# Kernel optimization log

Measured on AMD Instinct MI355X. Metric: run time of the kernel, lower is better.

Reference implementation:

```python
import jax, jax.numpy as jnp
import numpy as np

N = 1024  # hidden_state
L = 16384  # sequence length


def setup_inputs() -> dict:
    key = jax.random.key(0)
    kA, kB, kC, kd, kX = jax.random.split(key, 5)
    # kaiming_normal_ with nonlinearity='linear': std = 1/sqrt(fan_in) = 1/sqrt(N)
    A = jax.random.normal(kA, (N, N), dtype=jnp.float32) / jnp.sqrt(jnp.float32(N))
    # nn.init.normal_(B, std=(1/N)**0.5)
    B = jax.random.normal(kB, (N, 1), dtype=jnp.float32) / jnp.sqrt(jnp.float32(N))
    # nn.init.normal_(C, std=1.0)
    C = jax.random.normal(kC, (1, N), dtype=jnp.float32)
    D = jnp.ones((1,), dtype=jnp.float32)
    # uniform in [log(min_delta), log(max_delta)]
    log_delta = jax.random.uniform(kd, (1,), dtype=jnp.float32,
                                   minval=jnp.log(1e-3), maxval=jnp.log(1e-1))
    X = jax.random.normal(kX, (L,), dtype=jnp.float32)
    return {"X": X, "A": A, "B": B, "C": C, "D": D, "log_delta": log_delta}


def _discretize(A, B, log_delta):
    n = A.shape[0]
    I = jnp.eye(n, dtype=A.dtype)
    d = jnp.exp(log_delta)  # (1,) broadcasts
    A1 = I - d * 0.5 * A
    A2 = I + d * 0.5 * A
    A1_inv = jnp.linalg.inv(A1)
    dA = A1_inv @ A2                 # (N, N) bilinear (Tustin) discretization
    dB = (A1_inv @ (d * B))[:, 0]    # (N,)
    return dA, dB


def reference(X, A, B, C, D, log_delta):
    """S4 RNN-mode forward: linear state-space recurrence + skip connection."""
    dA, dB = _discretize(A, B, log_delta)
    c = C[0]  # (N,)

    def step(h, x):
        # h_k = dA @ h_{k-1} + dB * x_k ; y_k = C @ h_k
        h = dA @ h + dB * x
        return h, c @ h

    h0 = jnp.zeros((A.shape[0],), dtype=A.dtype)  # cache_h_k starts at zeros
    _, ys = jax.lax.scan(step, h0, X)             # ys: (L,)
    return ys + D * X                              # skip = D * X
```

## Files before the change

### kernel.cpp

```cpp
#include <hip/hip_runtime.h>
#include <math.h>

#define N1 1024
#define NN2 (N1*N1)
#define LL 16384

__global__ __launch_bounds__(256) void k_scale(const float* __restrict__ A,
                                               const float* __restrict__ logd,
                                               float* __restrict__ e) {
    int i = blockIdx.x * 256 + threadIdx.x;
    float d = expf(logd[0]);
    e[i] = 0.5f * d * A[i];
}

__global__ __launch_bounds__(256) void k_add(const float* __restrict__ a,
                                             const float* __restrict__ b,
                                             float* __restrict__ o) {
    int i = blockIdx.x * 256 + threadIdx.x;
    o[i] = a[i] + b[i];
}

__global__ __launch_bounds__(256) void k_mmk(const float* __restrict__ A,
                                             const float* __restrict__ B,
                                             float* __restrict__ part) {
    __shared__ float As[32][68];
    __shared__ float Bs[32][68];
    int t = threadIdx.x;
    int m0 = blockIdx.y * 64, n0 = blockIdx.x * 64;
    int kz = blockIdx.z * 512;
    int tm = (t & 15) * 4, tn = (t >> 4) * 4;
    int lmA = t >> 2, lkA = (t & 3) * 8;
    int kbB = t >> 3, nbB = (t & 7) * 8;
    const float* Ap = A + (size_t)(m0 + lmA) * N1 + kz + lkA;
    const float* Bp = B + (size_t)(kz + kbB) * N1 + n0 + nbB;

    float4 pa0 = *(const float4*)(Ap);
    float4 pa1 = *(const float4*)(Ap + 4);
    float4 pb0 = *(const float4*)(Bp);
    float4 pb1 = *(const float4*)(Bp + 4);

    float acc[4][4];
#pragma unroll
    for (int i = 0; i < 4; ++i)
#pragma unroll
        for (int j = 0; j < 4; ++j) acc[i][j] = 0.f;

    for (int k0 = 0; k0 < 512; k0 += 32) {
        As[lkA + 0][lmA] = pa0.x; As[lkA + 1][lmA] = pa0.y;
        As[lkA + 2][lmA] = pa0.z; As[lkA + 3][lmA] = pa0.w;
        As[lkA + 4][lmA] = pa1.x; As[lkA + 5][lmA] = pa1.y;
        As[lkA + 6][lmA] = pa1.z; As[lkA + 7][lmA] = pa1.w;
        *(float4*)&Bs[kbB][nbB]     = pb0;
        *(float4*)&Bs[kbB][nbB + 4] = pb1;
        __syncthreads();
        if (k0 + 32 < 512) {
            pa0 = *(const float4*)(Ap + k0 + 32);
            pa1 = *(const float4*)(Ap + k0 + 36);
            pb0 = *(const float4*)(Bp + (size_t)(k0 + 32) * N1);
            pb1 = *(const float4*)(Bp + (size_t)(k0 + 32) * N1 + 4);
        }
#pragma unroll
        for (int k = 0; k < 32; ++k) {
            float4 a = *(float4*)&As[k][tm];
            float4 b = *(float4*)&Bs[k][tn];
            acc[0][0] += a.x * b.x; acc[0][1] += a.x * b.y; acc[0][2] += a.x * b.z; acc[0][3] += a.x * b.w;
            acc[1][0] += a.y * b.x; acc[1][1] += a.y * b.y; acc[1][2] += a.y * b.z; acc[1][3] += a.y * b.w;
            acc[2][0] += a.z * b.x; acc[2][1] += a.z * b.y; acc[2][2] += a.z * b.z; acc[2][3] += a.z * b.w;
            acc[3][0] += a.w * b.x; acc[3][1] += a.w * b.y; acc[3][2] += a.w * b.z; acc[3][3] += a.w * b.w;
        }
        __syncthreads();
    }
    float* Po = part + (size_t)blockIdx.z * NN2;
#pragma unroll
    for (int i = 0; i < 4; ++i) {
        float4 o = {acc[i][0], acc[i][1], acc[i][2], acc[i][3]};
        *(float4*)&Po[(size_t)(m0 + tm + i) * N1 + n0 + tn] = o;
    }
}

__global__ __launch_bounds__(256) void k_mmred(const float* __restrict__ part,
                                               const float* __restrict__ Aadd,
                                               float* __restrict__ C,
                                               float alpha, float beta) {
    int i = (blockIdx.x * 256 + threadIdx.x) * 4;
    float4 p0 = *(const float4*)&part[i];
    float4 p1 = *(const float4*)&part[NN2 + i];
    float4 av = *(const float4*)&Aadd[i];
    float4 o;
    o.x = alpha * (p0.x + p1.x) + beta * av.x;
    o.y = alpha * (p0.y + p1.y) + beta * av.y;
    o.z = alpha * (p0.z + p1.z) + beta * av.z;
    o.w = alpha * (p0.w + p1.w) + beta * av.w;
    *(float4*)&C[i] = o;
}

__global__ __launch_bounds__(256) void k_chainQ1(const float* __restrict__ M,
                                                 const float* __restrict__ V,
                                                 float* __restrict__ part,
                                                 int kc, int mlen) {
    __shared__ float Vs[256];
    int i = blockIdx.z, t = threadIdx.x;
    int n0 = blockIdx.x * 64, m0 = blockIdx.y * mlen;
    const float* Vi = V + (size_t)i * N1 + m0;
    if (t * 4 < mlen) *(float4*)&Vs[t * 4] = *(const float4*)&Vi[t * 4];
    __syncthreads();
    int wave = t >> 6, lane = t & 63;
    for (int rr = 0; rr < 16; ++rr) {
        int n = n0 + wave * 16 + rr;
        const float* Mr = M + (size_t)n * N1 + m0;
        float acc = 0.f;
        for (int m = lane * 4; m < mlen; m += 256) {
            float4 a = *(const float4*)&Mr[m];
            float4 v = *(const float4*)&Vs[m];
            acc += a.x * v.x + a.y * v.y + a.z * v.z + a.w * v.w;
        }
#pragma unroll
        for (int off = 32; off > 0; off >>= 1) acc += __shfl_down(acc, off, 64);
        if (lane == 0) part[((size_t)i * kc + blockIdx.y) * N1 + n] = acc;
    }
}

__global__ __launch_bounds__(256) void k_chainP1(const float* __restrict__ M,
                                                 const float* __restrict__ P,
                                                 float* __restrict__ part,
                                                 int kc, int mlen) {
    __shared__ float Ps[256];
    __shared__ float red[4][64];
    int i = blockIdx.z, t = threadIdx.x;
    int n0 = blockIdx.x * 64, m0 = blockIdx.y * mlen;
    const float* Pi = P + (size_t)i * N1 + m0;
    if (t * 4 < mlen) *(float4*)&Ps[t * 4] = *(const float4*)&Pi[t * 4];
    __syncthreads();
    int wave = t >> 6, lane = t & 63;
    int n = n0 + lane;
    int msub = mlen >> 2;
    int mb = wave * msub;
    float acc = 0.f;
#pragma unroll 8
    for (int m = 0; m < msub; ++m)
        acc += Ps[mb + m] * M[(size_t)(m0 + mb + m) * N1 + n];
    red[wave][lane] = acc;
    __syncthreads();
    if (t < 64) {
        float s = red[0][t] + red[1][t] + red[2][t] + red[3][t];
        part[((size_t)i * kc + blockIdx.y) * N1 + n0 + t] = s;
    }
}

__global__ __launch_bounds__(256) void k_chainR(float* __restrict__ V,
                                                const float* __restrict__ part,
                                                int w, int kc) {
    int i = blockIdx.y, t = threadIdx.x;
    int n = blockIdx.x * 256 + t;
    const float* pp = part + (size_t)i * kc * N1 + n;
    float s = 0.f;
    for (int c = 0; c < kc; ++c) s += pp[(size_t)c * N1];
    V[(size_t)(w + i) * N1 + n] = V[(size_t)i * N1 + n] + s;
}

__global__ __launch_bounds__(256) void k_initR(const float* __restrict__ Bv,
                                               const float* __restrict__ Cv,
                                               const float* __restrict__ logd,
                                               const float* __restrict__ part,
                                               float* __restrict__ Q,
                                               float* __restrict__ P) {
    int n = blockIdx.x * 256 + threadIdx.x;
    float s = 0.f;
    for (int c = 0; c < 16; ++c) s += part[(size_t)c * N1 + n];
    float d = expf(logd[0]);
    Q[n] = d * (Bv[n] + 0.5f * s);
    P[n] = Cv[n];
}

__global__ __launch_bounds__(256) void k_kdot(const float* __restrict__ P,
                                              const float* __restrict__ Q,
                                              float* __restrict__ K) {
    int t = threadIdx.x;
    int wid = blockIdx.x * 4 + (t >> 6), lane = t & 63;
    int a = wid >> 7, b = wid & 127;
    const float* Pr = P + (size_t)a * N1;
    const float* Qr = Q + (size_t)b * N1;
    float acc = 0.f;
#pragma unroll
    for (int jj = 0; jj < 4; ++jj) {
        int m = jj * 256 + lane * 4;
        float4 p = *(const float4*)&Pr[m];
        float4 q = *(const float4*)&Qr[m];
        acc += p.x * q.x + p.y * q.y + p.z * q.z + p.w * q.w;
    }
#pragma unroll
    for (int off = 32; off > 0; off >>= 1) acc += __shfl_down(acc, off, 64);
    if (lane == 0) K[wid] = acc;
}

__global__ __launch_bounds__(256) void k_conv1(const float* __restrict__ X,
                                               const float* __restrict__ K,
                                               float* __restrict__ part) {
    __shared__ __align__(16) float ks[1280];
    __shared__ __align__(16) float xs[256];
    int bx = blockIdx.x, tt = threadIdx.x;
    int o = 0;
    while (bx >= 2 * (o + 1) * (o + 1) + 2 * (o + 1)) ++o;
    int jt = bx - (2 * o * o + 2 * o);
    int T0 = o * 1024, J0 = jt * 256;
    int mb = T0 - J0 - 255;
    for (int ii = tt; ii < 1280; ii += 256) {
        int m = mb + ii;
        ks[ii] = (m >= 0 && m < LL) ? K[m] : 0.f;
    }
    xs[tt] = X[J0 + tt];
    __syncthreads();

    float acc0 = 0.f, acc1 = 0.f, acc2 = 0.f, acc3 = 0.f;
    int base0 = 4 * tt + 252;
#pragma unroll 4
    for (int jj = 0; jj < 256; jj += 4) {
        float4 xv  = *(const float4*)&xs[jj];
        float4 kv0 = *(const float4*)&ks[base0 - jj];
        float4 kv1 = *(const float4*)&ks[base0 - jj + 4];
        float kk0 = kv0.x, kk1 = kv0.y, kk2 = kv0.z, kk3 = kv0.w;
        float kk4 = kv1.x, kk5 = kv1.y, kk6 = kv1.z;
        acc0 += kk3 * xv.x + kk2 * xv.y + kk1 * xv.z + kk0 * xv.w;
        acc1 += kk4 * xv.x + kk3 * xv.y + kk2 * xv.z + kk1 * xv.w;
        acc2 += kk5 * xv.x + kk4 * xv.y + kk3 * xv.z + kk2 * xv.w;
        acc3 += kk6 * xv.x + kk5 * xv.y + kk4 * xv.z + kk3 * xv.w;
    }
    float4 out = {acc0, acc1, acc2, acc3};
    *(float4*)&part[((size_t)(o * 64 + jt)) * 1024 + 4 * tt] = out;
}

__global__ __launch_bounds__(256) void k_conv2(const float* __restrict__ X,
                                               const float* __restrict__ part,
                                               const float* __restrict__ Dp,
                                               float* __restrict__ Y) {
    int o = blockIdx.x, tt = threadIdx.x;
    int c = 4 * tt;
    float s0 = 0.f, s1 = 0.f, s2 = 0.f, s3 = 0.f;
    int cnt = 4 * o + 4;
    for (int jt = 0; jt < cnt; ++jt) {
        float4 p = *(const float4*)&part[((size_t)(o * 64 + jt)) * 1024 + c];
        s0 += p.x; s1 += p.y; s2 += p.z; s3 += p.w;
    }
    float dsk = Dp[0];
    int t = o * 1024 + c;
    float4 xv = *(const float4*)&X[t];
    float4 out;
    out.x = dsk * xv.x + s0;
    out.y = dsk * xv.y + s1;
    out.z = dsk * xv.z + s2;
    out.w = dsk * xv.w + s3;
    *(float4*)&Y[t] = out;
}

extern "C" void kernel_launch(void* const* d_in, const int* in_sizes, int n_in,
                              void* d_out, int out_size, void* d_ws, size_t ws_size,
                              hipStream_t stream) {
    const float* X    = (const float*)d_in[0];
    const float* A    = (const float*)d_in[1];
    const float* Bv   = (const float*)d_in[2];
    const float* Cv   = (const float*)d_in[3];
    const float* Dp   = (const float*)d_in[4];
    const float* logd = (const float*)d_in[5];
    float* ws = (float*)d_ws;

    float* S0 = ws;
    float* S1 = ws + (size_t)NN2;
    float* S2 = ws + 2*(size_t)NN2;
    float* S3 = ws + 3*(size_t)NN2;
    float* S4 = ws + 4*(size_t)NN2;
    float* MP = ws + 5*(size_t)NN2;
    float* CP = MP + (size_t)NN2;
    float* Q  = ws + 7*(size_t)NN2;
    float* P  = Q + 128*(size_t)N1;
    float* Kc = P + 128*(size_t)N1;
    float* Y  = (float*)d_out;

    dim3 mmg(16, 16, 2);

#define MM(Ain, Bin, Cout, al, be) \
    k_mmk<<<mmg, 256, 0, stream>>>(Ain, Bin, MP); \
    k_mmred<<<1024, 256, 0, stream>>>(MP, Ain, Cout, al, be);

    k_scale<<<4096, 256, 0, stream>>>(A, logd, S0);
    MM(S0, S0, S1, 1.f, 0.f);
    MM(S1, S1, S2, 1.f, 1.f);
    k_add<<<4096, 256, 0, stream>>>(S0, S1, S3);
    MM(S3, S2, S4, 2.f, 2.f);

    k_chainQ1<<<dim3(16, 16, 1), 256, 0, stream>>>(S4, Bv, CP, 16, 64);
    k_initR<<<4, 256, 0, stream>>>(Bv, Cv, logd, CP, Q, P);

    float* cur = S4;
    float* nxt = S0;
    for (int k = 0; k < 7; ++k) {
        int w = 1 << k;
        int kc = (w == 1) ? 16 : (w <= 4 ? 8 : 4);
        k_chainQ1<<<dim3(16, kc, w), 256, 0, stream>>>(cur, Q, CP, kc, N1 / kc);
        k_chainR<<<dim3(4, w), 256, 0, stream>>>(Q, CP, w, kc);
        MM(cur, cur, nxt, 1.f, 2.f);
        float* tsw = cur; cur = nxt; nxt = tsw;
    }
    for (int k = 0; k < 7; ++k) {
        int w = 1 << k;
        int kc = (w == 1) ? 16 : (w <= 4 ? 8 : 4);
        k_chainP1<<<dim3(16, kc, w), 256, 0, stream>>>(cur, P, CP, kc, N1 / kc);
        k_chainR<<<dim3(4, w), 256, 0, stream>>>(P, CP, w, kc);
        if (k < 6) {
            MM(cur, cur, nxt, 1.f, 2.f);
            float* tsw = cur; cur = nxt; nxt = tsw;
        }
    }
    k_kdot<<<4096, 256, 0, stream>>>(P, Q, Kc);
    k_conv1<<<544, 256, 0, stream>>>(X, Kc, MP);
    k_conv2<<<16, 256, 0, stream>>>(X, MP, Dp, Y);
#undef MM
}
```

Measured before the change: 887.9 us.

## Fuse chain matvec blocks into matmul launches and double-buffer GEMM LDS

```diff
diff --git a/kernel.cpp b/kernel.cpp
--- a/kernel.cpp
+++ b/kernel.cpp
@@ -20,24 +20,93 @@
     o[i] = a[i] + b[i];
 }
 
-__global__ __launch_bounds__(256) void k_mmk(const float* __restrict__ A,
-                                             const float* __restrict__ B,
-                                             float* __restrict__ part) {
-    __shared__ float As[32][68];
-    __shared__ float Bs[32][68];
+__device__ __forceinline__ void chain_part(const float* __restrict__ M,
+                                           float* __restrict__ V,
+                                           float* __restrict__ CP,
+                                           int w, int lkc, int mode, int cb,
+                                           float* sV, float (*red)[64]) {
+    int kc = 1 << lkc;
+    int i = cb >> (4 + lkc);
+    int ky = (cb >> 4) & (kc - 1);
+    int nx = cb & 15;
+    int mlen = N1 >> lkc;
+    int m0 = ky * mlen, n0 = nx * 64;
     int t = threadIdx.x;
-    int m0 = blockIdx.y * 64, n0 = blockIdx.x * 64;
-    int kz = blockIdx.z * 512;
+    const float* Vi = V + (size_t)i * N1 + m0;
+    if (t * 4 < mlen) *(float4*)&sV[t * 4] = *(const float4*)&Vi[t * 4];
+    __syncthreads();
+    int wave = t >> 6, lane = t & 63;
+    if (mode == 0) {
+        for (int rr = 0; rr < 16; ++rr) {
+            int n = n0 + wave * 16 + rr;
+            const float* Mr = M + (size_t)n * N1 + m0;
+            float acc = 0.f;
+            for (int m = lane * 4; m < mlen; m += 256) {
+                float4 a = *(const float4*)&Mr[m];
+                float4 v = *(const float4*)&sV[m];
+                acc += a.x * v.x + a.y * v.y + a.z * v.z + a.w * v.w;
+            }
+#pragma unroll
+            for (int off = 32; off > 0; off >>= 1) acc += __shfl_down(acc, off, 64);
+            if (lane == 0) {
+                if (kc == 1) V[(size_t)(w + i) * N1 + n] = sV[n] + acc;
+                else CP[((size_t)i * kc + ky) * N1 + n] = acc;
+            }
+        }
+    } else {
+        int n = n0 + lane;
+        int msub = mlen >> 2;
+        int mb = wave * msub;
+        float acc = 0.f;
+#pragma unroll 8
+        for (int m = 0; m < msub; ++m)
+            acc += sV[mb + m] * M[(size_t)(m0 + mb + m) * N1 + n];
+        red[wave][lane] = acc;
+        __syncthreads();
+        if (t < 64) {
+            float s = red[0][t] + red[1][t] + red[2][t] + red[3][t];
+            if (kc == 1) V[(size_t)(w + i) * N1 + n0 + t] = sV[n0 + t] + s;
+            else CP[((size_t)i * kc + ky) * N1 + n0 + t] = s;
+        }
+    }
+}
+
+__global__ __launch_bounds__(256) void k_fused(const float* __restrict__ Ain,
+                                               const float* __restrict__ Bin,
+                                               float* __restrict__ part,
+                                               float* __restrict__ V,
+                                               float* __restrict__ CP,
+                                               int w, int lkc, int nchain, int mode) {
+    __shared__ float As[2][32][68];
+    __shared__ float Bs[2][32][68];
+    __shared__ float sV[N1];
+    __shared__ float red[4][64];
+    int b = blockIdx.x;
+    if (b < nchain) {
+        chain_part(Ain, V, CP, w, lkc, mode, b, sV, red);
+        return;
+    }
+    int g = b - nchain;
+    int t = threadIdx.x;
+    int z = g >> 8, ty = (g >> 4) & 15, tx = g & 15;
+    int m0 = ty * 64, n0 = tx * 64, kz = z * 512;
     int tm = (t & 15) * 4, tn = (t >> 4) * 4;
     int lmA = t >> 2, lkA = (t & 3) * 8;
     int kbB = t >> 3, nbB = (t & 7) * 8;
-    const float* Ap = A + (size_t)(m0 + lmA) * N1 + kz + lkA;
-    const float* Bp = B + (size_t)(kz + kbB) * N1 + n0 + nbB;
+    const float* Ap = Ain + (size_t)(m0 + lmA) * N1 + kz + lkA;
+    const float* Bp = Bin + (size_t)(kz + kbB) * N1 + n0 + nbB;
 
     float4 pa0 = *(const float4*)(Ap);
     float4 pa1 = *(const float4*)(Ap + 4);
     float4 pb0 = *(const float4*)(Bp);
     float4 pb1 = *(const float4*)(Bp + 4);
+    As[0][lkA + 0][lmA] = pa0.x; As[0][lkA + 1][lmA] = pa0.y;
+    As[0][lkA + 2][lmA] = pa0.z; As[0][lkA + 3][lmA] = pa0.w;
+    As[0][lkA + 4][lmA] = pa1.x; As[0][lkA + 5][lmA] = pa1.y;
+    As[0][lkA + 6][lmA] = pa1.z; As[0][lkA + 7][lmA] = pa1.w;
+    *(float4*)&Bs[0][kbB][nbB]     = pb0;
+    *(float4*)&Bs[0][kbB][nbB + 4] = pb1;
+    __syncthreads();
 
     float acc[4][4];
 #pragma unroll
@@ -45,32 +114,37 @@
 #pragma unroll
         for (int j = 0; j < 4; ++j) acc[i][j] = 0.f;
 
-    for (int k0 = 0; k0 < 512; k0 += 32) {
-        As[lkA + 0][lmA] = pa0.x; As[lkA + 1][lmA] = pa0.y;
-        As[lkA + 2][lmA] = pa0.z; As[lkA + 3][lmA] = pa0.w;
-        As[lkA + 4][lmA] = pa1.x; As[lkA + 5][lmA] = pa1.y;
-        As[lkA + 6][lmA] = pa1.z; As[lkA + 7][lmA] = pa1.w;
-        *(float4*)&Bs[kbB][nbB]     = pb0;
-        *(float4*)&Bs[kbB][nbB + 4] = pb1;
-        __syncthreads();
-        if (k0 + 32 < 512) {
-            pa0 = *(const float4*)(Ap + k0 + 32);
-            pa1 = *(const float4*)(Ap + k0 + 36);
-            pb0 = *(const float4*)(Bp + (size_t)(k0 + 32) * N1);
-            pb1 = *(const float4*)(Bp + (size_t)(k0 + 32) * N1 + 4);
+    for (int tt = 0; tt < 16; ++tt) {
+        int cur = tt & 1;
+        float4 na0, na1, nb0, nb1;
+        if (tt < 15) {
+            int k0 = (tt + 1) * 32;
+            na0 = *(const float4*)(Ap + k0);
+            na1 = *(const float4*)(Ap + k0 + 4);
+            nb0 = *(const float4*)(Bp + (size_t)k0 * N1);
+            nb1 = *(const float4*)(Bp + (size_t)k0 * N1 + 4);
         }
 #pragma unroll
         for (int k = 0; k < 32; ++k) {
-            float4 a = *(float4*)&As[k][tm];
-            float4 b = *(float4*)&Bs[k][tn];
-            acc[0][0] += a.x * b.x; acc[0][1] += a.x * b.y; acc[0][2] += a.x * b.z; acc[0][3] += a.x * b.w;
-            acc[1][0] += a.y * b.x; acc[1][1] += a.y * b.y; acc[1][2] += a.y * b.z; acc[1][3] += a.y * b.w;
-            acc[2][0] += a.z * b.x; acc[2][1] += a.z * b.y; acc[2][2] += a.z * b.z; acc[2][3] += a.z * b.w;
-            acc[3][0] += a.w * b.x; acc[3][1] += a.w * b.y; acc[3][2] += a.w * b.z; acc[3][3] += a.w * b.w;
-        }
-        __syncthreads();
-    }
-    float* Po = part + (size_t)blockIdx.z * NN2;
+            float4 a = *(float4*)&As[cur][k][tm];
+            float4 bb = *(float4*)&Bs[cur][k][tn];
+            acc[0][0] += a.x * bb.x; acc[0][1] += a.x * bb.y; acc[0][2] += a.x * bb.z; acc[0][3] += a.x * bb.w;
+            acc[1][0] += a.y * bb.x; acc[1][1] += a.y * bb.y; acc[1][2] += a.y * bb.z; acc[1][3] += a.y * bb.w;
+            acc[2][0] += a.z * bb.x; acc[2][1] += a.z * bb.y; acc[2][2] += a.z * bb.z; acc[2][3] += a.z * bb.w;
+            acc[3][0] += a.w * bb.x; acc[3][1] += a.w * bb.y; acc[3][2] += a.w * bb.z; acc[3][3] += a.w * bb.w;
+        }
+        if (tt < 15) {
+            int nxt = cur ^ 1;
+            As[nxt][lkA + 0][lmA] = na0.x; As[nxt][lkA + 1][lmA] = na0.y;
+            As[nxt][lkA + 2][lmA] = na0.z; As[nxt][lkA + 3][lmA] = na0.w;
+            As[nxt][lkA + 4][lmA] = na1.x; As[nxt][lkA + 5][lmA] = na1.y;
+            As[nxt][lkA + 6][lmA] = na1.z; As[nxt][lkA + 7][lmA] = na1.w;
+            *(float4*)&Bs[nxt][kbB][nbB]     = nb0;
+            *(float4*)&Bs[nxt][kbB][nbB + 4] = nb1;
+            __syncthreads();
+        }
+    }
+    float* Po = part + (size_t)z * NN2;
 #pragma unroll
     for (int i = 0; i < 4; ++i) {
         float4 o = {acc[i][0], acc[i][1], acc[i][2], acc[i][3]};
@@ -78,84 +152,43 @@
     }
 }
 
-__global__ __launch_bounds__(256) void k_mmred(const float* __restrict__ part,
-                                               const float* __restrict__ Aadd,
-                                               float* __restrict__ C,
-                                               float alpha, float beta) {
-    int i = (blockIdx.x * 256 + threadIdx.x) * 4;
-    float4 p0 = *(const float4*)&part[i];
-    float4 p1 = *(const float4*)&part[NN2 + i];
-    float4 av = *(const float4*)&Aadd[i];
-    float4 o;
-    o.x = alpha * (p0.x + p1.x) + beta * av.x;
-    o.y = alpha * (p0.y + p1.y) + beta * av.y;
-    o.z = alpha * (p0.z + p1.z) + beta * av.z;
-    o.w = alpha * (p0.w + p1.w) + beta * av.w;
-    *(float4*)&C[i] = o;
-}
-
-__global__ __launch_bounds__(256) void k_chainQ1(const float* __restrict__ M,
-                                                 const float* __restrict__ V,
-                                                 float* __restrict__ part,
-                                                 int kc, int mlen) {
-    __shared__ float Vs[256];
-    int i = blockIdx.z, t = threadIdx.x;
-    int n0 = blockIdx.x * 64, m0 = blockIdx.y * mlen;
-    const float* Vi = V + (size_t)i * N1 + m0;
-    if (t * 4 < mlen) *(float4*)&Vs[t * 4] = *(const float4*)&Vi[t * 4];
-    __syncthreads();
-    int wave = t >> 6, lane = t & 63;
-    for (int rr = 0; rr < 16; ++rr) {
-        int n = n0 + wave * 16 + rr;
-        const float* Mr = M + (size_t)n * N1 + m0;
-        float acc = 0.f;
-        for (int m = lane * 4; m < mlen; m += 256) {
-            float4 a = *(const float4*)&Mr[m];
-            float4 v = *(const float4*)&Vs[m];
-            acc += a.x * v.x + a.y * v.y + a.z * v.z + a.w * v.w;
-        }
-#pragma unroll
-        for (int off = 32; off > 0; off >>= 1) acc += __shfl_down(acc, off, 64);
-        if (lane == 0) part[((size_t)i * kc + blockIdx.y) * N1 + n] = acc;
-    }
-}
-
-__global__ __launch_bounds__(256) void k_chainP1(const float* __restrict__ M,
-                                                 const float* __restrict__ P,
-                                                 float* __restrict__ part,
-                                                 int kc, int mlen) {
-    __shared__ float Ps[256];
+__global__ __launch_bounds__(256) void k_cpart(const float* __restrict__ M,
+                                               float* __restrict__ V,
+                                               float* __restrict__ CP,
+                                               int w, int lkc, int mode) {
+    __shared__ float sV[N1];
     __shared__ float red[4][64];
-    int i = blockIdx.z, t = threadIdx.x;
-    int n0 = blockIdx.x * 64, m0 = blockIdx.y * mlen;
-    const float* Pi = P + (size_t)i * N1 + m0;
-    if (t * 4 < mlen) *(float4*)&Ps[t * 4] = *(const float4*)&Pi[t * 4];
-    __syncthreads();
-    int wave = t >> 6, lane = t & 63;
-    int n = n0 + lane;
-    int msub = mlen >> 2;
-    int mb = wave * msub;
-    float acc = 0.f;
-#pragma unroll 8
-    for (int m = 0; m < msub; ++m)
-        acc += Ps[mb + m] * M[(size_t)(m0 + mb + m) * N1 + n];
-    red[wave][lane] = acc;
-    __syncthreads();
-    if (t < 64) {
-        float s = red[0][t] + red[1][t] + red[2][t] + red[3][t];
-        part[((size_t)i * kc + blockIdx.y) * N1 + n0 + t] = s;
-    }
-}
-
-__global__ __launch_bounds__(256) void k_chainR(float* __restrict__ V,
-                                                const float* __restrict__ part,
-                                                int w, int kc) {
-    int i = blockIdx.y, t = threadIdx.x;
-    int n = blockIdx.x * 256 + t;
-    const float* pp = part + (size_t)i * kc * N1 + n;
-    float s = 0.f;
-    for (int c = 0; c < kc; ++c) s += pp[(size_t)c * N1];
-    V[(size_t)(w + i) * N1 + n] = V[(size_t)i * N1 + n] + s;
+    chain_part(M, V, CP, w, lkc, mode, blockIdx.x, sV, red);
+}
+
+__global__ __launch_bounds__(256) void k_redu(const float* __restrict__ part,
+                                              const float* __restrict__ Aadd,
+                                              float* __restrict__ C,
+                                              float alpha, float beta,
+                                              float* __restrict__ V,
+                                              const float* __restrict__ CP,
+                                              int w, int kc) {
+    int b = blockIdx.x, t = threadIdx.x;
+    if (b < 1024) {
+        int i = (b * 256 + t) * 4;
+        float4 p0 = *(const float4*)&part[i];
+        float4 p1 = *(const float4*)&part[NN2 + i];
+        float4 av = *(const float4*)&Aadd[i];
+        float4 o;
+        o.x = alpha * (p0.x + p1.x) + beta * av.x;
+        o.y = alpha * (p0.y + p1.y) + beta * av.y;
+        o.z = alpha * (p0.z + p1.z) + beta * av.z;
+        o.w = alpha * (p0.w + p1.w) + beta * av.w;
+        *(float4*)&C[i] = o;
+    } else {
+        int rb = b - 1024;
+        int i = rb >> 2;
+        int n = (rb & 3) * 256 + t;
+        const float* pp = CP + (size_t)i * kc * N1 + n;
+        float s = 0.f;
+        for (int c = 0; c < kc; ++c) s += pp[(size_t)c * N1];
+        V[(size_t)(w + i) * N1 + n] = V[(size_t)i * N1 + n] + s;
+    }
 }
 
 __global__ __launch_bounds__(256) void k_initR(const float* __restrict__ Bv,
@@ -269,49 +302,49 @@
     float* S3 = ws + 3*(size_t)NN2;
     float* S4 = ws + 4*(size_t)NN2;
     float* MP = ws + 5*(size_t)NN2;
-    float* CP = MP + (size_t)NN2;
-    float* Q  = ws + 7*(size_t)NN2;
+    float* CP = ws + 7*(size_t)NN2;
+    float* Q  = CP + 64*(size_t)N1;
     float* P  = Q + 128*(size_t)N1;
     float* Kc = P + 128*(size_t)N1;
     float* Y  = (float*)d_out;
 
-    dim3 mmg(16, 16, 2);
-
-#define MM(Ain, Bin, Cout, al, be) \
-    k_mmk<<<mmg, 256, 0, stream>>>(Ain, Bin, MP); \
-    k_mmred<<<1024, 256, 0, stream>>>(MP, Ain, Cout, al, be);
-
     k_scale<<<4096, 256, 0, stream>>>(A, logd, S0);
-    MM(S0, S0, S1, 1.f, 0.f);
-    MM(S1, S1, S2, 1.f, 1.f);
+    k_fused<<<512, 256, 0, stream>>>(S0, S0, MP, nullptr, nullptr, 0, 0, 0, 0);
+    k_redu<<<1024, 256, 0, stream>>>(MP, S0, S1, 1.f, 0.f, nullptr, nullptr, 0, 0);
+    k_fused<<<512, 256, 0, stream>>>(S1, S1, MP, nullptr, nullptr, 0, 0, 0, 0);
+    k_redu<<<1024, 256, 0, stream>>>(MP, S1, S2, 1.f, 1.f, nullptr, nullptr, 0, 0);
     k_add<<<4096, 256, 0, stream>>>(S0, S1, S3);
-    MM(S3, S2, S4, 2.f, 2.f);
-
-    k_chainQ1<<<dim3(16, 16, 1), 256, 0, stream>>>(S4, Bv, CP, 16, 64);
+    k_fused<<<512, 256, 0, stream>>>(S3, S2, MP, nullptr, nullptr, 0, 0, 0, 0);
+    k_redu<<<1024, 256, 0, stream>>>(MP, S3, S4, 2.f, 2.f, nullptr, nullptr, 0, 0);
+
+    k_cpart<<<256, 256, 0, stream>>>(S4, (float*)Bv, CP, 1, 4, 0);
     k_initR<<<4, 256, 0, stream>>>(Bv, Cv, logd, CP, Q, P);
 
     float* cur = S4;
     float* nxt = S0;
     for (int k = 0; k < 7; ++k) {
         int w = 1 << k;
-        int kc = (w == 1) ? 16 : (w <= 4 ? 8 : 4);
-        k_chainQ1<<<dim3(16, kc, w), 256, 0, stream>>>(cur, Q, CP, kc, N1 / kc);
-        k_chainR<<<dim3(4, w), 256, 0, stream>>>(Q, CP, w, kc);
-        MM(cur, cur, nxt, 1.f, 2.f);
+        int lkc = (w < 16) ? (4 - k) : 0;
+        int kc = 1 << lkc;
+        int nchain = 16 * kc * w;
+        int nR = (kc > 1) ? 4 * w : 0;
+        k_fused<<<nchain + 512, 256, 0, stream>>>(cur, cur, MP, Q, CP, w, lkc, nchain, 0);
+        k_redu<<<1024 + nR, 256, 0, stream>>>(MP, cur, nxt, 1.f, 2.f, Q, CP, w, kc);
         float* tsw = cur; cur = nxt; nxt = tsw;
     }
-    for (int k = 0; k < 7; ++k) {
+    for (int k = 0; k < 6; ++k) {
         int w = 1 << k;
-        int kc = (w == 1) ? 16 : (w <= 4 ? 8 : 4);
-        k_chainP1<<<dim3(16, kc, w), 256, 0, stream>>>(cur, P, CP, kc, N1 / kc);
-        k_chainR<<<dim3(4, w), 256, 0, stream>>>(P, CP, w, kc);
-        if (k < 6) {
-            MM(cur, cur, nxt, 1.f, 2.f);
-            float* tsw = cur; cur = nxt; nxt = tsw;
-        }
-    }
+        int lkc = (w < 16) ? (4 - k) : 0;
+        int kc = 1 << lkc;
+        int nchain = 16 * kc * w;
+        int nR = (kc > 1) ? 4 * w : 0;
+        k_fused<<<nchain + 512, 256, 0, stream>>>(cur, cur, MP, P, CP, w, lkc, nchain, 1);
+        k_redu<<<1024 + nR, 256, 0, stream>>>(MP, cur, nxt, 1.f, 2.f, P, CP, w, kc);
+        float* tsw = cur; cur = nxt; nxt = tsw;
+    }
+    k_cpart<<<1024, 256, 0, stream>>>(cur, P, CP, 64, 0, 1);
+
     k_kdot<<<4096, 256, 0, stream>>>(P, Q, Kc);
     k_conv1<<<544, 256, 0, stream>>>(X, Kc, MP);
     k_conv2<<<16, 256, 0, stream>>>(X, MP, Dp, Y);
-#undef MM
-}
+}
```

Result: faster. 795.7 us (-10.4%).
